# Kernel optimization log

Measured on AMD Instinct MI355X. Metric: run time of the kernel, lower is better.

The kernel has to match this reference:

```python
import jax, jax.numpy as jnp
import numpy as np

IN_FEATURES = 1024
OUT_FEATURES = 1024
NUM_GMM = 5
MAX_STD = 3.0
ROWS = (IN_FEATURES + 1) * OUT_FEATURES  # (in+1)*out rows of GMM params


def setup_inputs() -> dict:
    key = jax.random.key(0)
    kx, km, kl, kw = jax.random.split(key, 4)
    x = jax.random.normal(kx, (4096, IN_FEATURES), dtype=jnp.float32)
    mean = jax.random.normal(km, (ROWS, NUM_GMM), dtype=jnp.float32)
    logstd = jax.random.normal(kl, (ROWS, NUM_GMM), dtype=jnp.float32)
    weight = jax.random.normal(kw, (ROWS, NUM_GMM), dtype=jnp.float32)
    return {"x": x, "mean": mean, "logstd": logstd, "weight": weight}


def reference(x, mean, logstd, weight):
    # GMM weight sampling: Categorical(softmax(weight)) picks a component per row,
    # then Normal(mean_sel, exp(tanh(logstd_sel)*max_std)) is sampled.
    key = jax.random.key(42)
    kcat, knorm = jax.random.split(key)
    # categorical with logits == Categorical(probs=softmax(weight))
    idx = jax.random.categorical(kcat, weight, axis=-1)  # [ROWS] int
    sel_mean = jnp.take_along_axis(mean, idx[:, None], axis=1)[:, 0]      # [ROWS]
    sel_logstd = jnp.take_along_axis(logstd, idx[:, None], axis=1)[:, 0]  # [ROWS]
    sel_std = jnp.exp(jnp.tanh(sel_logstd) * MAX_STD)
    eps = jax.random.normal(knorm, (mean.shape[0],), dtype=mean.dtype)
    weight_bias = sel_mean + sel_std * eps  # torch .sample() -> no grad flow
    weight_bias = jax.lax.stop_gradient(weight_bias)
    bias = weight_bias[:OUT_FEATURES]                                   # [out]
    W = weight_bias[OUT_FEATURES:].reshape(OUT_FEATURES, IN_FEATURES)   # [out, in]
    return x @ W.T + bias
```

## Files before the change

kernel.cpp:

```cpp
#include <hip/hip_runtime.h>
#include <cstdint>
#include <cmath>

#define IN_FEATURES 1024
#define OUT_FEATURES 1024
#define NUM_GMM 5
#define ROWS ((IN_FEATURES + 1) * OUT_FEATURES)

struct U2 { uint32_t a, b; };

__host__ __device__ constexpr uint32_t rotl32c(uint32_t x, int d) {
  return (x << d) | (x >> (32 - d));
}

#define TF_ROUND(r) { x0 += x1; x1 = rotl32c(x1, (r)); x1 ^= x0; }
__host__ __device__ constexpr U2 threefry2x32(uint32_t k0, uint32_t k1,
                                              uint32_t x0, uint32_t x1) {
  const uint32_t ks0 = k0, ks1 = k1, ks2 = k0 ^ k1 ^ 0x1BD11BDAu;
  x0 += ks0; x1 += ks1;
  TF_ROUND(13) TF_ROUND(15) TF_ROUND(26) TF_ROUND(6)
  x0 += ks1; x1 += ks2 + 1u;
  TF_ROUND(17) TF_ROUND(29) TF_ROUND(16) TF_ROUND(24)
  x0 += ks2; x1 += ks0 + 2u;
  TF_ROUND(13) TF_ROUND(15) TF_ROUND(26) TF_ROUND(6)
  x0 += ks0; x1 += ks1 + 3u;
  TF_ROUND(17) TF_ROUND(29) TF_ROUND(16) TF_ROUND(24)
  x0 += ks1; x1 += ks2 + 4u;
  TF_ROUND(13) TF_ROUND(15) TF_ROUND(26) TF_ROUND(6)
  x0 += ks2; x1 += ks0 + 5u;
  return U2{x0, x1};
}

constexpr U2 KC = threefry2x32(0u, 42u, 0u, 0u);
constexpr U2 KN = threefry2x32(0u, 42u, 0u, 1u);
constexpr uint32_t KCAT0  = KC.a;
constexpr uint32_t KCAT1  = KC.b;
constexpr uint32_t KNORM0 = KN.a;
constexpr uint32_t KNORM1 = KN.b;

__device__ inline float u01_from_bits(uint32_t bits) {
  return __uint_as_float((bits >> 9) | 0x3F800000u) - 1.0f;
}

__device__ inline float log_f32_acc(float x) {
  uint32_t ix = __float_as_uint(x);
  int e = (int)(ix >> 23) - 127;
  float mf = __uint_as_float((ix & 0x007FFFFFu) | 0x3F800000u);
  if (mf > 1.4142135381698608f) { mf *= 0.5f; e += 1; }
  double m = (double)mf;
  double d = m + 1.0;
  double r = (double)__builtin_amdgcn_rcpf((float)d);
  r = r * (2.0 - d * r);
  r = r * (2.0 - d * r);
  double t = (m - 1.0) * r;
  double t2 = t * t;
  double p = 1.0 / 15.0;
  p = fma(p, t2, 1.0 / 13.0);
  p = fma(p, t2, 1.0 / 11.0);
  p = fma(p, t2, 1.0 / 9.0);
  p = fma(p, t2, 1.0 / 7.0);
  p = fma(p, t2, 1.0 / 5.0);
  p = fma(p, t2, 1.0 / 3.0);
  p = fma(p, t2, 1.0);
  double res = fma((double)e, 0.693147180559945309417, 2.0 * t * p);
  return (float)res;
}

__device__ inline float u_from_bits_clamped(uint32_t bits) {
  float f = u01_from_bits(bits);
  return fmaxf(1.17549435e-38f, f + 1.17549435e-38f);
}

__device__ inline float gumbel_acc(uint32_t bits) {
  float u = u_from_bits_clamped(bits);
  float t1 = log_f32_acc(u);
  float t2 = log_f32_acc(-t1);
  return -t2;
}

__device__ inline float gumbel_fast(uint32_t bits) {
  float u = u_from_bits_clamped(bits);
  float t1 = __logf(u);
  return -__logf(-t1);
}

__device__ inline float erfinv_xla(float x) {
  float s = (1.0f - x) * (1.0f + x);
  float w = -__logf(s);
  float p;
  if (w < 5.0f) {
    w = w - 2.5f;
    p = 2.81022636e-08f;
    p = fmaf(p, w, 3.43273939e-07f);
    p = fmaf(p, w, -3.5233877e-06f);
    p = fmaf(p, w, -4.39150654e-06f);
    p = fmaf(p, w, 0.00021858087f);
    p = fmaf(p, w, -0.00125372503f);
    p = fmaf(p, w, -0.00417768164f);
    p = fmaf(p, w, 0.246640727f);
    p = fmaf(p, w, 1.50140941f);
  } else {
    w = sqrtf(w) - 3.0f;
    p = -0.000200214257f;
    p = fmaf(p, w, 0.000100950558f);
    p = fmaf(p, w, 0.00134934322f);
    p = fmaf(p, w, -0.00367342844f);
    p = fmaf(p, w, 0.00573950773f);
    p = fmaf(p, w, -0.0076224613f);
    p = fmaf(p, w, 0.00943887047f);
    p = fmaf(p, w, 1.00167406f);
    p = fmaf(p, w, 2.83297682f);
  }
  return p * x;
}

__device__ inline float normal_from_bits(uint32_t bits) {
  float f = u01_from_bits(bits);
  const float lo = -0.99999994f;
  float u = fmaxf(lo, f * 2.0f + lo);
  return 1.4142135623730951f * erfinv_xla(u);
}

__device__ inline unsigned short f32_to_bf16_rne(float f) {
  uint32_t u = __float_as_uint(f);
  return (unsigned short)((u + 0x7FFFu + ((u >> 16) & 1u)) >> 16);
}

__global__ __launch_bounds__(256) void prep_kernel(
    const float* __restrict__ mean, const float* __restrict__ logstd,
    const float* __restrict__ weight, const float* __restrict__ x,
    unsigned short* __restrict__ wh, float* __restrict__ bias_f32,
    unsigned short* __restrict__ xh, int n_chunks) {
  const int r = blockIdx.x * 256 + threadIdx.x;

  if (r < n_chunks) {
    int i = r * 8;
    float4 a = *(const float4*)(x + i);
    float4 b = *(const float4*)(x + i + 4);
    union { unsigned short s[8]; uint4 v; } o;
    o.s[0] = f32_to_bf16_rne(a.x); o.s[1] = f32_to_bf16_rne(a.y);
    o.s[2] = f32_to_bf16_rne(a.z); o.s[3] = f32_to_bf16_rne(a.w);
    o.s[4] = f32_to_bf16_rne(b.x); o.s[5] = f32_to_bf16_rne(b.y);
    o.s[6] = f32_to_bf16_rne(b.z); o.s[7] = f32_to_bf16_rne(b.w);
    *(uint4*)(xh + i) = o.v;
  }

  const float* wrow = weight + (size_t)r * NUM_GMM;
  uint32_t bits[NUM_GMM];
  float wv[NUM_GMM];
  float v[NUM_GMM];
#pragma unroll
  for (int g = 0; g < NUM_GMM; ++g) {
    U2 t = threefry2x32(KCAT0, KCAT1, 0u, (uint32_t)(r * NUM_GMM + g));
    bits[g] = t.a ^ t.b;
    wv[g] = wrow[g];
    v[g] = gumbel_fast(bits[g]) + wv[g];
  }
  int idx = 0;
  float best = v[0], second = -3.402823466e+38f;
#pragma unroll
  for (int g = 1; g < NUM_GMM; ++g) {
    if (v[g] > best) { second = best; best = v[g]; idx = g; }
    else if (v[g] > second) { second = v[g]; }
  }
  if (__builtin_expect(best - second < 1e-3f, 0)) {
    idx = 0;
    best = -3.402823466e+38f;
#pragma unroll
    for (int g = 0; g < NUM_GMM; ++g) {
      float va = gumbel_acc(bits[g]) + wv[g];
      if (va > best) { best = va; idx = g; }
    }
  }

  U2 tn = threefry2x32(KNORM0, KNORM1, 0u, (uint32_t)r);
  float eps = normal_from_bits(tn.a ^ tn.b);

  float m = mean[(size_t)r * NUM_GMM + idx];
  float l = logstd[(size_t)r * NUM_GMM + idx];
  float e2 = __expf(2.0f * l);
  float th = 1.0f - 2.0f * __builtin_amdgcn_rcpf(e2 + 1.0f);
  float sd = __expf(3.0f * th);
  float wbv = m + sd * eps;
  wh[r] = f32_to_bf16_rne(wbv);
  if (r < OUT_FEATURES) bias_f32[r] = wbv;
}

typedef __attribute__((ext_vector_type(8))) short bf16x8;
typedef __attribute__((ext_vector_type(4))) float f32x4;

#define GBM 128
#define GBN 64
#define GBK 64

__device__ inline void load_lds16(const void* g, void* l) {
  __builtin_amdgcn_global_load_lds(
      (const __attribute__((address_space(1))) unsigned int*)g,
      (__attribute__((address_space(3))) unsigned int*)l, 16, 0, 0);
}

__global__ __launch_bounds__(256) void gemm_mfma_kernel(
    const unsigned short* __restrict__ xh, const unsigned short* __restrict__ wh,
    const float* __restrict__ bias, float* __restrict__ out) {
  __shared__ unsigned short As[3][GBM * GBK];
  __shared__ unsigned short Bs[3][GBN * GBK];

  const unsigned short* W = wh + OUT_FEATURES;
  const int tid = threadIdx.x;
  const int w = tid >> 6;
  const int L = tid & 63;

  const int m_tile = blockIdx.y * GBM;
  const int n_tile = blockIdx.x * GBN;

  const int sm = tid & 15;
  const int sh = (tid >> 4) & 3;
  const int sk = (tid >> 6) & 1;
  const int sb = tid >> 7;
  const int kofs = sk * 32 + sh * 8;

  const unsigned short* gA[4];
  const unsigned short* gB[2];
#pragma unroll
  for (int i = 0; i < 4; ++i)
    gA[i] = xh + (size_t)(m_tile + (2 * i + sb) * 16 + sm) * IN_FEATURES + kofs;
#pragma unroll
  for (int i = 0; i < 2; ++i)
    gB[i] = W + (size_t)(n_tile + (2 * i + sb) * 16 + sm) * IN_FEATURES + kofs;

  f32x4 acc[2][4];
#pragma unroll
  for (int a = 0; a < 2; ++a)
#pragma unroll
    for (int b = 0; b < 4; ++b) acc[a][b] = (f32x4){0.f, 0.f, 0.f, 0.f};

#define STAGE(buf, k0)                                                    \
  {                                                                       \
    _Pragma("unroll")                                                     \
    for (int i = 0; i < 4; ++i)                                           \
      load_lds16(gA[i] + (k0), &As[buf][(size_t)(tid + 256 * i) * 8]);    \
    _Pragma("unroll")                                                     \
    for (int i = 0; i < 2; ++i)                                           \
      load_lds16(gB[i] + (k0), &Bs[buf][(size_t)(tid + 256 * i) * 8]);    \
  }

  STAGE(0, 0)
  STAGE(1, GBK)

  const int NK = IN_FEATURES / GBK;
#pragma unroll
  for (int kt = 0; kt < NK; ++kt) {
    asm volatile("s_waitcnt vmcnt(6)" ::: "memory");
    asm volatile("s_barrier" ::: "memory");
    if (kt + 2 < NK) STAGE((kt + 2) % 3, (kt + 2) * GBK)
    const unsigned short* Ab = As[kt % 3];
    const unsigned short* Bb = Bs[kt % 3];
#pragma unroll
    for (int s = 0; s < 2; ++s) {
      bf16x8 a0 = *(const bf16x8*)(Ab + (((2 * w + 0) * 2 + s) * 64 + L) * 8);
      bf16x8 a1 = *(const bf16x8*)(Ab + (((2 * w + 1) * 2 + s) * 64 + L) * 8);
      bf16x8 b0 = *(const bf16x8*)(Bb + ((0 * 2 + s) * 64 + L) * 8);
      bf16x8 b1 = *(const bf16x8*)(Bb + ((1 * 2 + s) * 64 + L) * 8);
      bf16x8 b2 = *(const bf16x8*)(Bb + ((2 * 2 + s) * 64 + L) * 8);
      bf16x8 b3 = *(const bf16x8*)(Bb + ((3 * 2 + s) * 64 + L) * 8);
      acc[0][0] = __builtin_amdgcn_mfma_f32_16x16x32_bf16(a0, b0, acc[0][0], 0, 0, 0);
      acc[0][1] = __builtin_amdgcn_mfma_f32_16x16x32_bf16(a0, b1, acc[0][1], 0, 0, 0);
      acc[0][2] = __builtin_amdgcn_mfma_f32_16x16x32_bf16(a0, b2, acc[0][2], 0, 0, 0);
      acc[0][3] = __builtin_amdgcn_mfma_f32_16x16x32_bf16(a0, b3, acc[0][3], 0, 0, 0);
      acc[1][0] = __builtin_amdgcn_mfma_f32_16x16x32_bf16(a1, b0, acc[1][0], 0, 0, 0);
      acc[1][1] = __builtin_amdgcn_mfma_f32_16x16x32_bf16(a1, b1, acc[1][1], 0, 0, 0);
      acc[1][2] = __builtin_amdgcn_mfma_f32_16x16x32_bf16(a1, b2, acc[1][2], 0, 0, 0);
      acc[1][3] = __builtin_amdgcn_mfma_f32_16x16x32_bf16(a1, b3, acc[1][3], 0, 0, 0);
    }
  }

  const int colL = L & 15;
  const int rowq = (L >> 4) * 4;
  float bv[4];
#pragma unroll
  for (int nb = 0; nb < 4; ++nb) bv[nb] = bias[n_tile + nb * 16 + colL];
#pragma unroll
  for (int bm = 0; bm < 2; ++bm) {
#pragma unroll
    for (int reg = 0; reg < 4; ++reg) {
      int row = m_tile + w * 32 + bm * 16 + rowq + reg;
#pragma unroll
      for (int nb = 0; nb < 4; ++nb) {
        out[(size_t)row * OUT_FEATURES + n_tile + nb * 16 + colL] =
            acc[bm][nb][reg] + bv[nb];
      }
    }
  }
}

extern "C" void kernel_launch(void* const* d_in, const int* in_sizes, int n_in,
                              void* d_out, int out_size, void* d_ws, size_t ws_size,
                              hipStream_t stream) {
  const float* x      = (const float*)d_in[0];
  const float* mean   = (const float*)d_in[1];
  const float* logstd = (const float*)d_in[2];
  const float* weight = (const float*)d_in[3];
  float* out = (float*)d_out;

  const int M = in_sizes[0] / IN_FEATURES;

  unsigned short* xh = (unsigned short*)d_ws;
  unsigned short* wh = (unsigned short*)((char*)d_ws + (size_t)M * IN_FEATURES * 2);
  float* biasf = (float*)((char*)wh + (size_t)ROWS * 2);

  const int n_chunks = M * IN_FEATURES / 8;
  prep_kernel<<<ROWS / 256, 256, 0, stream>>>(
      mean, logstd, weight, x, wh, biasf, xh, n_chunks);

  dim3 grid(OUT_FEATURES / GBN, M / GBM);
  gemm_mfma_kernel<<<grid, 256, 0, stream>>>(xh, wh, biasf, out);
}
```

Before: 139.9 us.

## Enlarge GEMM tile to 128x128 with XCD-aware block mapping and hoist GMM loads

Result: faster. 133.9 us (-4.3%).

```diff
diff --git a/kernel.cpp b/kernel.cpp
--- a/kernel.cpp
+++ b/kernel.cpp
@@ -133,6 +133,17 @@
     unsigned short* __restrict__ xh, int n_chunks) {
   const int r = blockIdx.x * 256 + threadIdx.x;
 
+  const float* wrow = weight + (size_t)r * NUM_GMM;
+  const float* mrow = mean   + (size_t)r * NUM_GMM;
+  const float* lrow = logstd + (size_t)r * NUM_GMM;
+  float wv[NUM_GMM], mv[NUM_GMM], lv[NUM_GMM];
+#pragma unroll
+  for (int g = 0; g < NUM_GMM; ++g) {
+    wv[g] = wrow[g];
+    mv[g] = mrow[g];
+    lv[g] = lrow[g];
+  }
+
   if (r < n_chunks) {
     int i = r * 8;
     float4 a = *(const float4*)(x + i);
@@ -145,15 +156,12 @@
     *(uint4*)(xh + i) = o.v;
   }
 
-  const float* wrow = weight + (size_t)r * NUM_GMM;
   uint32_t bits[NUM_GMM];
-  float wv[NUM_GMM];
   float v[NUM_GMM];
 #pragma unroll
   for (int g = 0; g < NUM_GMM; ++g) {
     U2 t = threefry2x32(KCAT0, KCAT1, 0u, (uint32_t)(r * NUM_GMM + g));
     bits[g] = t.a ^ t.b;
-    wv[g] = wrow[g];
     v[g] = gumbel_fast(bits[g]) + wv[g];
   }
   int idx = 0;
@@ -176,8 +184,13 @@
   U2 tn = threefry2x32(KNORM0, KNORM1, 0u, (uint32_t)r);
   float eps = normal_from_bits(tn.a ^ tn.b);
 
-  float m = mean[(size_t)r * NUM_GMM + idx];
-  float l = logstd[(size_t)r * NUM_GMM + idx];
+  float m = mv[0], l = lv[0];
+#pragma unroll
+  for (int g = 1; g < NUM_GMM; ++g) {
+    bool sel = (idx == g);
+    m = sel ? mv[g] : m;
+    l = sel ? lv[g] : l;
+  }
   float e2 = __expf(2.0f * l);
   float th = 1.0f - 2.0f * __builtin_amdgcn_rcpf(e2 + 1.0f);
   float sd = __expf(3.0f * th);
@@ -190,7 +203,7 @@
 typedef __attribute__((ext_vector_type(4))) float f32x4;
 
 #define GBM 128
-#define GBN 64
+#define GBN 128
 #define GBK 64
 
 __device__ inline void load_lds16(const void* g, void* l) {
@@ -209,9 +222,14 @@
   const int tid = threadIdx.x;
   const int w = tid >> 6;
   const int L = tid & 63;
-
-  const int m_tile = blockIdx.y * GBM;
-  const int n_tile = blockIdx.x * GBN;
+  const int wr = w >> 1;
+  const int wc = w & 1;
+
+  const int lin = blockIdx.x;
+  const int xcd = lin & 7;
+  const int loc = lin >> 3;
+  const int m_tile = ((xcd >> 1) * 8 + (loc >> 2)) * GBM;
+  const int n_tile = ((xcd & 1) * 4 + (loc & 3)) * GBN;
 
   const int sm = tid & 15;
   const int sh = (tid >> 4) & 3;
@@ -220,17 +238,17 @@
   const int kofs = sk * 32 + sh * 8;
 
   const unsigned short* gA[4];
-  const unsigned short* gB[2];
+  const unsigned short* gB[4];
 #pragma unroll
   for (int i = 0; i < 4; ++i)
     gA[i] = xh + (size_t)(m_tile + (2 * i + sb) * 16 + sm) * IN_FEATURES + kofs;
 #pragma unroll
-  for (int i = 0; i < 2; ++i)
+  for (int i = 0; i < 4; ++i)
     gB[i] = W + (size_t)(n_tile + (2 * i + sb) * 16 + sm) * IN_FEATURES + kofs;
 
-  f32x4 acc[2][4];
-#pragma unroll
-  for (int a = 0; a < 2; ++a)
+  f32x4 acc[4][4];
+#pragma unroll
+  for (int a = 0; a < 4; ++a)
 #pragma unroll
     for (int b = 0; b < 4; ++b) acc[a][b] = (f32x4){0.f, 0.f, 0.f, 0.f};
 
@@ -240,7 +258,7 @@
     for (int i = 0; i < 4; ++i)                                           \
       load_lds16(gA[i] + (k0), &As[buf][(size_t)(tid + 256 * i) * 8]);    \
     _Pragma("unroll")                                                     \
-    for (int i = 0; i < 2; ++i)                                           \
+    for (int i = 0; i < 4; ++i)                                           \
       load_lds16(gB[i] + (k0), &Bs[buf][(size_t)(tid + 256 * i) * 8]);    \
   }
 
@@ -250,27 +268,30 @@
   const int NK = IN_FEATURES / GBK;
 #pragma unroll
   for (int kt = 0; kt < NK; ++kt) {
-    asm volatile("s_waitcnt vmcnt(6)" ::: "memory");
+    if (kt < NK - 1) {
+      asm volatile("s_waitcnt vmcnt(8)" ::: "memory");
+    } else {
+      asm volatile("s_waitcnt vmcnt(0)" ::: "memory");
+    }
     asm volatile("s_barrier" ::: "memory");
     if (kt + 2 < NK) STAGE((kt + 2) % 3, (kt + 2) * GBK)
     const unsigned short* Ab = As[kt % 3];
     const unsigned short* Bb = Bs[kt % 3];
 #pragma unroll
     for (int s = 0; s < 2; ++s) {
-      bf16x8 a0 = *(const bf16x8*)(Ab + (((2 * w + 0) * 2 + s) * 64 + L) * 8);
-      bf16x8 a1 = *(const bf16x8*)(Ab + (((2 * w + 1) * 2 + s) * 64 + L) * 8);
-      bf16x8 b0 = *(const bf16x8*)(Bb + ((0 * 2 + s) * 64 + L) * 8);
-      bf16x8 b1 = *(const bf16x8*)(Bb + ((1 * 2 + s) * 64 + L) * 8);
-      bf16x8 b2 = *(const bf16x8*)(Bb + ((2 * 2 + s) * 64 + L) * 8);
-      bf16x8 b3 = *(const bf16x8*)(Bb + ((3 * 2 + s) * 64 + L) * 8);
-      acc[0][0] = __builtin_amdgcn_mfma_f32_16x16x32_bf16(a0, b0, acc[0][0], 0, 0, 0);
-      acc[0][1] = __builtin_amdgcn_mfma_f32_16x16x32_bf16(a0, b1, acc[0][1], 0, 0, 0);
-      acc[0][2] = __builtin_amdgcn_mfma_f32_16x16x32_bf16(a0, b2, acc[0][2], 0, 0, 0);
-      acc[0][3] = __builtin_amdgcn_mfma_f32_16x16x32_bf16(a0, b3, acc[0][3], 0, 0, 0);
-      acc[1][0] = __builtin_amdgcn_mfma_f32_16x16x32_bf16(a1, b0, acc[1][0], 0, 0, 0);
-      acc[1][1] = __builtin_amdgcn_mfma_f32_16x16x32_bf16(a1, b1, acc[1][1], 0, 0, 0);
-      acc[1][2] = __builtin_amdgcn_mfma_f32_16x16x32_bf16(a1, b2, acc[1][2], 0, 0, 0);
-      acc[1][3] = __builtin_amdgcn_mfma_f32_16x16x32_bf16(a1, b3, acc[1][3], 0, 0, 0);
+      bf16x8 a[4], b[4];
+#pragma unroll
+      for (int m = 0; m < 4; ++m)
+        a[m] = *(const bf16x8*)(Ab + (((wr * 4 + m) * 2 + s) * 64 + L) * 8);
+#pragma unroll
+      for (int n = 0; n < 4; ++n)
+        b[n] = *(const bf16x8*)(Bb + (((wc * 4 + n) * 2 + s) * 64 + L) * 8);
+#pragma unroll
+      for (int m = 0; m < 4; ++m)
+#pragma unroll
+        for (int n = 0; n < 4; ++n)
+          acc[m][n] = __builtin_amdgcn_mfma_f32_16x16x32_bf16(
+              a[m], b[n], acc[m][n], 0, 0, 0);
     }
   }
 
@@ -278,16 +299,17 @@
   const int rowq = (L >> 4) * 4;
   float bv[4];
 #pragma unroll
-  for (int nb = 0; nb < 4; ++nb) bv[nb] = bias[n_tile + nb * 16 + colL];
-#pragma unroll
-  for (int bm = 0; bm < 2; ++bm) {
+  for (int nb = 0; nb < 4; ++nb)
+    bv[nb] = bias[n_tile + wc * 64 + nb * 16 + colL];
+#pragma unroll
+  for (int mb = 0; mb < 4; ++mb) {
 #pragma unroll
     for (int reg = 0; reg < 4; ++reg) {
-      int row = m_tile + w * 32 + bm * 16 + rowq + reg;
+      int row = m_tile + wr * 64 + mb * 16 + rowq + reg;
 #pragma unroll
       for (int nb = 0; nb < 4; ++nb) {
-        out[(size_t)row * OUT_FEATURES + n_tile + nb * 16 + colL] =
-            acc[bm][nb][reg] + bv[nb];
+        out[(size_t)row * OUT_FEATURES + n_tile + wc * 64 + nb * 16 + colL] =
+            acc[mb][nb][reg] + bv[nb];
       }
     }
   }
@@ -312,6 +334,6 @@
   prep_kernel<<<ROWS / 256, 256, 0, stream>>>(
       mean, logstd, weight, x, wh, biasf, xh, n_chunks);
 
-  dim3 grid(OUT_FEATURES / GBN, M / GBM);
+  dim3 grid((OUT_FEATURES / GBN) * (M / GBM));
   gemm_mfma_kernel<<<grid, 256, 0, stream>>>(xh, wh, biasf, out);
 }
```
